# Optimization experiments

Hardware: AMD Instinct MI355X
Metric: run time of the kernel (lower is better)

Reference implementation:

```python
import jax, jax.numpy as jnp
import numpy as np

N_NODES = 100000
N_EDGES = 1600000
D = 64  # in = hidden = out channels


def setup_inputs() -> dict:
    key = jax.random.key(0)
    ks = jax.random.split(key, 12)
    x = jax.random.normal(ks[0], (N_NODES, D), dtype=jnp.float32)
    src = jax.random.randint(ks[1], (N_EDGES,), 0, N_NODES, dtype=jnp.int32)
    dst = jax.random.randint(ks[2], (N_EDGES,), 0, N_NODES, dtype=jnp.int32)
    s = 1.0 / np.sqrt(D)
    params = {}
    for i in range(3):
        params[f"Wl{i}"] = jax.random.uniform(ks[3 + 3 * i], (D, D), jnp.float32, -s, s)
        params[f"bl{i}"] = jax.random.uniform(ks[4 + 3 * i], (D,), jnp.float32, -s, s)
        params[f"Wr{i}"] = jax.random.uniform(ks[5 + 3 * i], (D, D), jnp.float32, -s, s)
    return {"x": x, "src": src, "dst": dst, **params}


def _sage_conv(x, src, dst, Wl, bl, Wr):
    # mean aggregation of source-node features into destination nodes
    agg = jax.ops.segment_sum(x[src], dst, num_segments=N_NODES)          # [N, D]
    deg = jax.ops.segment_sum(jnp.ones((src.shape[0], 1), x.dtype), dst,
                              num_segments=N_NODES)                        # [N, 1]
    mean = agg / jnp.maximum(deg, 1.0)
    # PyG SAGEConv: lin_l(mean_neigh) + lin_r(x_root); lin_l has bias, lin_r does not
    return mean @ Wl.T + bl + x @ Wr.T


def reference(x, src, dst, Wl0, bl0, Wr0, Wl1, bl1, Wr1, Wl2, bl2, Wr2):
    h = jax.nn.relu(_sage_conv(x, src, dst, Wl0, bl0, Wr0))  # dropout no-op (eval)
    h = jax.nn.relu(_sage_conv(h, src, dst, Wl1, bl1, Wr1))
    return _sage_conv(h, src, dst, Wl2, bl2, Wr2)
```

## Files before the change

### kernel.cpp

```cpp
#include <hip/hip_runtime.h>

#define NN 100000
#define NE 1600000
#define D 64

#define NBUCK ((NN + 255) / 256)
#define EPB 4096
#define P1_BLOCKS ((NE + EPB - 1) / EPB)
#define BCAP 6144

#define F2BF_BLOCKS (NN * 16 / 256)
#define WPREP_BLOCKS (3 * 64 * 128 / 256)
#define ZERO_BLOCKS ((NBUCK + 255) / 256)

typedef __attribute__((ext_vector_type(8))) short bfrag;
typedef __attribute__((ext_vector_type(4))) float f4acc;

__device__ __forceinline__ unsigned short f2bf(float f) {
    unsigned u = __float_as_uint(f);
    u = (u + 0x7FFFu + ((u >> 16) & 1u)) >> 16;
    return (unsigned short)u;
}

__global__ __launch_bounds__(256) void prep_kernel(
    const float* __restrict__ x, unsigned short* __restrict__ xb,
    const float* __restrict__ Wl0, const float* __restrict__ Wr0,
    const float* __restrict__ Wl1, const float* __restrict__ Wr1,
    const float* __restrict__ Wl2, const float* __restrict__ Wr2,
    unsigned short* __restrict__ wcat, int* __restrict__ bucket_cur) {
    int b = blockIdx.x;
    int t = threadIdx.x;
    if (b < F2BF_BLOCKS) {
        int i = b * 256 + t;
        float4 v = ((const float4*)x)[i];
        ushort4 o;
        o.x = f2bf(v.x); o.y = f2bf(v.y); o.z = f2bf(v.z); o.w = f2bf(v.w);
        ((ushort4*)xb)[i] = o;
    } else if (b < F2BF_BLOCKS + WPREP_BLOCKS) {
        int i = (b - F2BF_BLOCKS) * 256 + t;
        int layer = i >> 13;
        int rem = i & 8191;
        int n = rem >> 7;
        int k = rem & 127;
        const float* W;
        if (layer == 0) W = (k < 64) ? Wl0 : Wr0;
        else if (layer == 1) W = (k < 64) ? Wl1 : Wr1;
        else W = (k < 64) ? Wl2 : Wr2;
        wcat[i] = f2bf(W[n * 64 + (k & 63)]);
    } else {
        int i = (b - F2BF_BLOCKS - WPREP_BLOCKS) * 256 + t;
        if (i < NBUCK) bucket_cur[i] = 0;
    }
}

__global__ __launch_bounds__(256) void p1_partition(const int* __restrict__ src,
                                                    const int* __restrict__ dst,
                                                    int* __restrict__ bucket_cur,
                                                    unsigned* __restrict__ packed, int nE) {
    __shared__ int h[NBUCK];
    __shared__ int ls[512];
    __shared__ int lstart[NBUCK];
    __shared__ int lcur[NBUCK];
    __shared__ unsigned sl[EPB];
    __shared__ unsigned short sb[EPB];
    int t = threadIdx.x;
    for (int i = t; i < NBUCK; i += 256) h[i] = 0;
    __syncthreads();
    int base = blockIdx.x * EPB;
    int cnt = min(EPB, nE - base);
    for (int i = t; i < cnt; i += 256) atomicAdd(&h[dst[base + i] >> 8], 1);
    __syncthreads();
    ls[t] = h[t];
    ls[t + 256] = (t + 256 < NBUCK) ? h[t + 256] : 0;
    __syncthreads();
    for (int off = 1; off < 512; off <<= 1) {
        int a = (t >= off) ? ls[t - off] : 0;
        int b2 = (t + 256 >= off) ? ls[t + 256 - off] : 0;
        __syncthreads();
        ls[t] += a;
        ls[t + 256] += b2;
        __syncthreads();
    }
    for (int i = t; i < NBUCK; i += 256) {
        int c = h[i];
        int excl = ls[i] - c;
        lstart[i] = excl;
        lcur[i] = excl;
        h[i] = c ? atomicAdd(&bucket_cur[i], c) : 0;
    }
    __syncthreads();
    for (int i = t; i < cnt; i += 256) {
        int d = dst[base + i];
        int bk = d >> 8;
        int pos = atomicAdd(&lcur[bk], 1);
        sl[pos] = ((unsigned)(d & 255) << 24) | (unsigned)src[base + i];
        sb[pos] = (unsigned short)bk;
    }
    __syncthreads();
    for (int j = t; j < cnt; j += 256) {
        int bk = sb[j];
        packed[bk * BCAP + h[bk] + (j - lstart[bk])] = sl[j];
    }
}

__global__ __launch_bounds__(256) void p2b_place(const unsigned* __restrict__ packed,
                                                 const int* __restrict__ bucket_cur,
                                                 int2* __restrict__ rowpair,
                                                 int* __restrict__ esrc, int nNodes) {
    __shared__ int h[256];
    __shared__ int cur[256];
    __shared__ int sl[BCAP];
    int b = blockIdx.x, t = threadIdx.x;
    h[t] = 0;
    __syncthreads();
    int lo = b * BCAP;
    int cnt = bucket_cur[b];
    for (int i = t; i < cnt; i += 256) atomicAdd(&h[packed[lo + i] >> 24], 1);
    __syncthreads();
    int v = h[t];
    for (int off = 1; off < 256; off <<= 1) {
        int u = (t >= off) ? h[t - off] : 0;
        __syncthreads();
        h[t] += u;
        __syncthreads();
    }
    int incl = h[t];
    int excl = incl - v;
    cur[t] = excl;
    int node = b * 256 + t;
    if (node < nNodes) rowpair[node] = make_int2(lo + excl, lo + incl);
    __syncthreads();
    for (int i = t; i < cnt; i += 256) {
        unsigned p = packed[lo + i];
        int pos = atomicAdd(&cur[p >> 24], 1);
        if (pos < BCAP) sl[pos] = (int)(p & 0xFFFFFFu);
    }
    __syncthreads();
    for (int i = t; i < cnt; i += 256) esrc[lo + i] = sl[i];
    if (t < 16 && cnt + t < BCAP) esrc[lo + cnt + t] = 0;
}

__global__ __launch_bounds__(256) void sage_layer(
    const unsigned short* __restrict__ xb,
    const int2* __restrict__ rowpair, const int* __restrict__ esrc,
    const unsigned short* __restrict__ wcat,
    const float* __restrict__ bl,
    float* __restrict__ outF,
    unsigned short* __restrict__ outB,
    int nNodes, int doRelu) {
    __shared__ unsigned short smean[32 * 64];

    int t = threadIdx.x;
    {
        int nl = t >> 3;
        int q = t & 7;
        int lane = t & 63;
        int gbase = lane & 56;
        int node = blockIdx.x * 32 + nl;
        uint4 o = make_uint4(0, 0, 0, 0);
        if (node < nNodes) {
            int2 rp = rowpair[node];
            int rs = rp.x;
            int re = rp.y;
            float a0 = 0, a1 = 0, a2 = 0, a3 = 0, a4 = 0, a5 = 0, a6 = 0, a7 = 0;
            for (int i = rs; i < re; i += 16) {
                int mA = esrc[i + q];
                int mB = esrc[i + 8 + q];
                int rem = re - i;
                int s[16];
#pragma unroll
                for (int j = 0; j < 16; ++j) {
                    int jj = min(j, rem - 1);
                    int sa = __shfl(mA, gbase + (jj & 7), 64);
                    int sb2 = __shfl(mB, gbase + (jj & 7), 64);
                    s[j] = (jj < 8) ? sa : sb2;
                }
#pragma unroll
                for (int j = 0; j < 16; ++j) {
                    uint4 w = ((const uint4*)xb)[s[j] * 8 + q];
                    if (i + j < re) {
                        a0 += __uint_as_float(w.x << 16);
                        a1 += __uint_as_float(w.x & 0xFFFF0000u);
                        a2 += __uint_as_float(w.y << 16);
                        a3 += __uint_as_float(w.y & 0xFFFF0000u);
                        a4 += __uint_as_float(w.z << 16);
                        a5 += __uint_as_float(w.z & 0xFFFF0000u);
                        a6 += __uint_as_float(w.w << 16);
                        a7 += __uint_as_float(w.w & 0xFFFF0000u);
                    }
                }
            }
            float inv = 1.0f / fmaxf((float)(re - rs), 1.0f);
            o.x = (unsigned)f2bf(a0 * inv) | ((unsigned)f2bf(a1 * inv) << 16);
            o.y = (unsigned)f2bf(a2 * inv) | ((unsigned)f2bf(a3 * inv) << 16);
            o.z = (unsigned)f2bf(a4 * inv) | ((unsigned)f2bf(a5 * inv) << 16);
            o.w = (unsigned)f2bf(a6 * inv) | ((unsigned)f2bf(a7 * inv) << 16);
        }
        int idx = nl * 64 + ((q * 8) ^ ((nl & 7) << 3));
        *(uint4*)&smean[idx] = o;
    }
    __syncthreads();

    int w = t >> 6;
    int l = t & 63;
    int lr = l & 15;
    int lk = l >> 4;

    const bfrag* wB = (const bfrag*)wcat;
    int n = w * 16 + lr;
    bfrag b0 = wB[n * 16 + lk];
    bfrag b1 = wB[n * 16 + 4 + lk];
    bfrag b2 = wB[n * 16 + 8 + lk];
    bfrag b3 = wB[n * 16 + 12 + lk];
    float bias = bl[n];

    int base = blockIdx.x * 32;
#pragma unroll
    for (int rt = 0; rt < 2; ++rt) {
        int row0 = base + rt * 16;
        int lrow = rt * 16 + lr;
        int sw = (lrow & 7) << 3;
        bfrag a0 = *(const bfrag*)&smean[lrow * 64 + ((lk * 8) ^ sw)];
        bfrag a1 = *(const bfrag*)&smean[lrow * 64 + ((32 + lk * 8) ^ sw)];
        int grow = row0 + lr;
        if (grow >= nNodes) grow = nNodes - 1;
        const bfrag* xr = (const bfrag*)(xb + (size_t)grow * D);
        bfrag a2 = xr[lk];
        bfrag a3 = xr[4 + lk];
        f4acc acc = {0.f, 0.f, 0.f, 0.f};
        acc = __builtin_amdgcn_mfma_f32_16x16x32_bf16(a0, b0, acc, 0, 0, 0);
        acc = __builtin_amdgcn_mfma_f32_16x16x32_bf16(a1, b1, acc, 0, 0, 0);
        acc = __builtin_amdgcn_mfma_f32_16x16x32_bf16(a2, b2, acc, 0, 0, 0);
        acc = __builtin_amdgcn_mfma_f32_16x16x32_bf16(a3, b3, acc, 0, 0, 0);
#pragma unroll
        for (int r = 0; r < 4; ++r) {
            int row = row0 + lk * 4 + r;
            if (row >= nNodes) continue;
            float v = acc[r] + bias;
            if (doRelu) v = fmaxf(v, 0.f);
            if (outF) outF[(size_t)row * D + n] = v;
            if (outB) outB[(size_t)row * D + n] = f2bf(v);
        }
    }
}

extern "C" void kernel_launch(void* const* d_in, const int* in_sizes, int n_in,
                              void* d_out, int out_size, void* d_ws, size_t ws_size,
                              hipStream_t stream) {
    const float* x   = (const float*)d_in[0];
    const int*   src = (const int*)d_in[1];
    const int*   dst = (const int*)d_in[2];
    const float* Wl0 = (const float*)d_in[3];
    const float* bl0 = (const float*)d_in[4];
    const float* Wr0 = (const float*)d_in[5];
    const float* Wl1 = (const float*)d_in[6];
    const float* bl1 = (const float*)d_in[7];
    const float* Wr1 = (const float*)d_in[8];
    const float* Wl2 = (const float*)d_in[9];
    const float* bl2 = (const float*)d_in[10];
    const float* Wr2 = (const float*)d_in[11];
    float* out = (float*)d_out;

    const size_t MB = 1 << 20;
    char* ws = (char*)d_ws;
    int* bucket_cur = (int*)(ws);
    unsigned short* wcat = (unsigned short*)(ws + (128 << 10));
    int2* rowpair = (int2*)(ws + 1 * MB);
    int* esrc   = (int*)(ws + 2 * MB);
    unsigned* packed = (unsigned*)(ws + 12 * MB);
    unsigned short* hbA = (unsigned short*)(ws + 12 * MB);
    unsigned short* xb  = (unsigned short*)(ws + 26 * MB);
    unsigned short* hbB = (unsigned short*)(ws + 39 * MB);

    prep_kernel<<<F2BF_BLOCKS + WPREP_BLOCKS + ZERO_BLOCKS, 256, 0, stream>>>(
        x, xb, Wl0, Wr0, Wl1, Wr1, Wl2, Wr2, wcat, bucket_cur);

    p1_partition<<<P1_BLOCKS, 256, 0, stream>>>(src, dst, bucket_cur, packed, NE);
    p2b_place<<<NBUCK, 256, 0, stream>>>(packed, bucket_cur, rowpair, esrc, NN);

    const int layerGrid = (NN + 31) / 32;
    sage_layer<<<layerGrid, 256, 0, stream>>>(xb,  rowpair, esrc, wcat,         bl0, nullptr, hbA, NN, 1);
    sage_layer<<<layerGrid, 256, 0, stream>>>(hbA, rowpair, esrc, wcat + 8192,  bl1, nullptr, hbB, NN, 1);
    sage_layer<<<layerGrid, 256, 0, stream>>>(hbB, rowpair, esrc, wcat + 16384, bl2, out, nullptr, NN, 0);
}
```

Measured before the change: 181.6 us.

## Fuse prep into partition kernel and stage layer outputs through LDS for coalesced stores

Merges the bf16 conversion and weight packing work into the edge-partition kernel as extra blocks, replacing the bucket-counter zeroing with a memset, so one launch and one serialization point go away. In the SAGE layer, MFMA results are written into a swizzled shared-memory tile and then stored row-wise with 16-byte vector writes instead of scattered 2- or 4-byte per-lane stores. This adds an extra shared buffer and barriers, and the prep blocks now share a launch with blocks that reserve large static shared memory, which may reduce occupancy for them.

```diff
diff --git a/kernel.cpp b/kernel.cpp
--- a/kernel.cpp
+++ b/kernel.cpp
@@ -11,7 +11,6 @@
 
 #define F2BF_BLOCKS (NN * 16 / 256)
 #define WPREP_BLOCKS (3 * 64 * 128 / 256)
-#define ZERO_BLOCKS ((NBUCK + 255) / 256)
 
 typedef __attribute__((ext_vector_type(8))) short bfrag;
 typedef __attribute__((ext_vector_type(4))) float f4acc;
@@ -22,52 +21,48 @@
     return (unsigned short)u;
 }
 
-__global__ __launch_bounds__(256) void prep_kernel(
+__global__ __launch_bounds__(256) void p1prep_kernel(
+    const int* __restrict__ src, const int* __restrict__ dst,
+    int* __restrict__ bucket_cur, unsigned* __restrict__ packed,
     const float* __restrict__ x, unsigned short* __restrict__ xb,
     const float* __restrict__ Wl0, const float* __restrict__ Wr0,
     const float* __restrict__ Wl1, const float* __restrict__ Wr1,
     const float* __restrict__ Wl2, const float* __restrict__ Wr2,
-    unsigned short* __restrict__ wcat, int* __restrict__ bucket_cur) {
+    unsigned short* __restrict__ wcat) {
     int b = blockIdx.x;
     int t = threadIdx.x;
-    if (b < F2BF_BLOCKS) {
-        int i = b * 256 + t;
-        float4 v = ((const float4*)x)[i];
-        ushort4 o;
-        o.x = f2bf(v.x); o.y = f2bf(v.y); o.z = f2bf(v.z); o.w = f2bf(v.w);
-        ((ushort4*)xb)[i] = o;
-    } else if (b < F2BF_BLOCKS + WPREP_BLOCKS) {
-        int i = (b - F2BF_BLOCKS) * 256 + t;
-        int layer = i >> 13;
-        int rem = i & 8191;
-        int n = rem >> 7;
-        int k = rem & 127;
-        const float* W;
-        if (layer == 0) W = (k < 64) ? Wl0 : Wr0;
-        else if (layer == 1) W = (k < 64) ? Wl1 : Wr1;
-        else W = (k < 64) ? Wl2 : Wr2;
-        wcat[i] = f2bf(W[n * 64 + (k & 63)]);
-    } else {
-        int i = (b - F2BF_BLOCKS - WPREP_BLOCKS) * 256 + t;
-        if (i < NBUCK) bucket_cur[i] = 0;
-    }
-}
-
-__global__ __launch_bounds__(256) void p1_partition(const int* __restrict__ src,
-                                                    const int* __restrict__ dst,
-                                                    int* __restrict__ bucket_cur,
-                                                    unsigned* __restrict__ packed, int nE) {
+    if (b >= P1_BLOCKS) {
+        int pb = b - P1_BLOCKS;
+        if (pb < F2BF_BLOCKS) {
+            int i = pb * 256 + t;
+            float4 v = ((const float4*)x)[i];
+            ushort4 o;
+            o.x = f2bf(v.x); o.y = f2bf(v.y); o.z = f2bf(v.z); o.w = f2bf(v.w);
+            ((ushort4*)xb)[i] = o;
+        } else {
+            int i = (pb - F2BF_BLOCKS) * 256 + t;
+            int layer = i >> 13;
+            int rem = i & 8191;
+            int n = rem >> 7;
+            int k = rem & 127;
+            const float* W;
+            if (layer == 0) W = (k < 64) ? Wl0 : Wr0;
+            else if (layer == 1) W = (k < 64) ? Wl1 : Wr1;
+            else W = (k < 64) ? Wl2 : Wr2;
+            wcat[i] = f2bf(W[n * 64 + (k & 63)]);
+        }
+        return;
+    }
     __shared__ int h[NBUCK];
     __shared__ int ls[512];
     __shared__ int lstart[NBUCK];
     __shared__ int lcur[NBUCK];
     __shared__ unsigned sl[EPB];
     __shared__ unsigned short sb[EPB];
-    int t = threadIdx.x;
     for (int i = t; i < NBUCK; i += 256) h[i] = 0;
     __syncthreads();
-    int base = blockIdx.x * EPB;
-    int cnt = min(EPB, nE - base);
+    int base = b * EPB;
+    int cnt = min(EPB, NE - base);
     for (int i = t; i < cnt; i += 256) atomicAdd(&h[dst[base + i] >> 8], 1);
     __syncthreads();
     ls[t] = h[t];
@@ -149,6 +144,7 @@
     unsigned short* __restrict__ outB,
     int nNodes, int doRelu) {
     __shared__ unsigned short smean[32 * 64];
+    __shared__ float tf[32 * 64];
 
     int t = threadIdx.x;
     {
@@ -215,6 +211,7 @@
     float bias = bl[n];
 
     int base = blockIdx.x * 32;
+    f4acc accv[2];
 #pragma unroll
     for (int rt = 0; rt < 2; ++rt) {
         int row0 = base + rt * 16;
@@ -232,14 +229,48 @@
         acc = __builtin_amdgcn_mfma_f32_16x16x32_bf16(a1, b1, acc, 0, 0, 0);
         acc = __builtin_amdgcn_mfma_f32_16x16x32_bf16(a2, b2, acc, 0, 0, 0);
         acc = __builtin_amdgcn_mfma_f32_16x16x32_bf16(a3, b3, acc, 0, 0, 0);
-#pragma unroll
-        for (int r = 0; r < 4; ++r) {
-            int row = row0 + lk * 4 + r;
-            if (row >= nNodes) continue;
-            float v = acc[r] + bias;
-            if (doRelu) v = fmaxf(v, 0.f);
-            if (outF) outF[(size_t)row * D + n] = v;
-            if (outB) outB[(size_t)row * D + n] = f2bf(v);
+        accv[rt] = acc;
+    }
+    __syncthreads();
+
+    if (outB) {
+#pragma unroll
+        for (int rt = 0; rt < 2; ++rt)
+#pragma unroll
+            for (int r = 0; r < 4; ++r) {
+                int row = rt * 16 + lk * 4 + r;
+                float v = accv[rt][r] + bias;
+                if (doRelu) v = fmaxf(v, 0.f);
+                smean[row * 64 + (n ^ ((row & 7) << 3))] = f2bf(v);
+            }
+        __syncthreads();
+        int row = t >> 3;
+        int node = base + row;
+        int c8 = t & 7;
+        if (node < nNodes) {
+            uint4 v = *(uint4*)&smean[row * 64 + ((c8 ^ (row & 7)) * 8)];
+            ((uint4*)outB)[(size_t)node * 8 + c8] = v;
+        }
+    } else {
+#pragma unroll
+        for (int rt = 0; rt < 2; ++rt)
+#pragma unroll
+            for (int r = 0; r < 4; ++r) {
+                int row = rt * 16 + lk * 4 + r;
+                float v = accv[rt][r] + bias;
+                if (doRelu) v = fmaxf(v, 0.f);
+                tf[row * 64 + (n ^ ((row & 7) << 3))] = v;
+            }
+        __syncthreads();
+        int row = t >> 3;
+        int node = base + row;
+        int c8 = t & 7;
+        if (node < nNodes) {
+            int cs = (c8 ^ (row & 7)) * 8;
+            float4 v0 = *(float4*)&tf[row * 64 + cs];
+            float4 v1 = *(float4*)&tf[row * 64 + cs + 4];
+            ((float4*)outF)[(size_t)node * 16 + c8 * 2 + 0] = v0;
+            ((float4*)outF)[(size_t)node * 16 + c8 * 2 + 1] = v1;
         }
     }
 }
@@ -272,10 +303,10 @@
     unsigned short* xb  = (unsigned short*)(ws + 26 * MB);
     unsigned short* hbB = (unsigned short*)(ws + 39 * MB);
 
-    prep_kernel<<<F2BF_BLOCKS + WPREP_BLOCKS + ZERO_BLOCKS, 256, 0, stream>>>(
-        x, xb, Wl0, Wr0, Wl1, Wr1, Wl2, Wr2, wcat, bucket_cur);
-
-    p1_partition<<<P1_BLOCKS, 256, 0, stream>>>(src, dst, bucket_cur, packed, NE);
+    hipMemsetAsync(bucket_cur, 0, (size_t)NBUCK * sizeof(int), stream);
+
+    p1prep_kernel<<<P1_BLOCKS + F2BF_BLOCKS + WPREP_BLOCKS, 256, 0, stream>>>(
+        src, dst, bucket_cur, packed, x, xb, Wl0, Wr0, Wl1, Wr1, Wl2, Wr2, wcat);
     p2b_place<<<NBUCK, 256, 0, stream>>>(packed, bucket_cur, rowpair, esrc, NN);
 
     const int layerGrid = (NN + 31) / 32;
```

New measurement: 177.5 us. -2.3%, faster.
